# Performance work log

Hardware: AMD Instinct MI355X
Metric: run time of the kernel (lower is better)

Reference implementation:

```python
import jax, jax.numpy as jnp
import numpy as np

T, D = 8192, 256   # frames, feature dim
P, K = 64, 128     # phone vocabulary, centers per phone


def setup_inputs() -> dict:
    key = jax.random.key(0)
    k1, k2, k3 = jax.random.split(key, 3)
    h = jax.random.normal(k1, (T, D), dtype=jnp.float32)
    centers = jax.random.normal(k2, (P, K, D), dtype=jnp.float32)
    phones = jax.random.randint(k3, (T,), 0, P, dtype=jnp.int64)
    return {"h": h, "centers": centers, "phones": phones}


def reference(h, centers, phones):
    """Per-phone 1-NN retrieval: for each frame t, find nearest center in the
    pool for phones[t] and return that center (anonymized feature).
    centers: [P, K, D] padded table replacing the (pattern, phone, gender) dict.
    """
    c = centers[phones]                                # [T, K, D] irregular gather
    # squared euclidean distance; ||h_t||^2 is constant per row -> omit for argmin
    d2 = jnp.sum(c * c, axis=-1) - 2.0 * jnp.einsum("td,tkd->tk", h, c)  # [T, K]
    idx = jnp.argmin(d2, axis=-1)                      # [T]
    h_anon = jnp.take_along_axis(c, idx[:, None, None], axis=1)[:, 0, :]  # [T, D]
    return h_anon
```

## Files before the change

kernel.cpp:

```cpp
#include <hip/hip_runtime.h>

#define T_FRAMES 8192
#define D_DIM    256
#define P_PHONES 64
#define K_CENT   128
#define TILE_F   32
#define MAX_SLOTS 1024

#define WS_NORMS  0
#define WS_FIDX   32768
#define WS_DESC   65536

__global__ __launch_bounds__(1024) void qr_prep_kernel(const float* __restrict__ centers,
                                                       const int* __restrict__ phones,
                                                       float* __restrict__ norms,
                                                       int* __restrict__ fidx,
                                                       int4* __restrict__ desc) {
    const int b   = blockIdx.x;
    const int tid = threadIdx.x;

    if (b > 0) {
        const int gwave = (b - 1) * 16 + (tid >> 6);
        const int lane  = tid & 63;
        const float4 cv = ((const float4*)(centers + (size_t)gwave * D_DIM))[lane];
        float s = cv.x * cv.x + cv.y * cv.y + cv.z * cv.z + cv.w * cv.w;
#pragma unroll
        for (int off = 32; off; off >>= 1) s += __shfl_xor(s, off, 64);
        if (lane == 0) norms[gwave] = s;
        return;
    }

    __shared__ int hist[P_PHONES];
    __shared__ int offp[P_PHONES];
    if (tid < P_PHONES) hist[tid] = 0;
    for (int i = tid; i < MAX_SLOTS; i += 1024) desc[i] = make_int4(0, 0, 0, 0);
    __syncthreads();
    for (int i = tid; i < T_FRAMES; i += 1024) atomicAdd(&hist[phones[i]], 1);
    __syncthreads();

    if (tid < 64) {
        const int c = hist[tid];
        int x = c;
#pragma unroll
        for (int off = 1; off < 64; off <<= 1) {
            int y = __shfl_up(x, off, 64);
            if (tid >= off) x += y;
        }
        const int fbase = x - c;
        offp[tid] = fbase;
        const int nt = (c + TILE_F - 1) / TILE_F;

        const int srcp = ((tid & 7) << 3) | (tid >> 3);
        const int ntq  = __shfl(nt, srcp, 64);
        int y2 = ntq;
#pragma unroll
        for (int off = 1; off < 64; off <<= 1) {
            int z = __shfl_up(y2, off, 64);
            if (tid >= off) y2 += z;
        }
        const int excl   = y2 - ntq;
        const int clbase = __shfl(excl, tid & 56, 64);
        const int within = excl - clbase;
        const int fb_q   = __shfl(fbase, srcp, 64);
        const int c_q    = __shfl(c, srcp, 64);
        const int r      = tid >> 3;
        for (int j = 0; j < ntq; ++j) {
            const int slot = r + 8 * (within + j);
            if (slot < MAX_SLOTS)
                desc[slot] = make_int4(srcp, fb_q + j * TILE_F,
                                       min(TILE_F, c_q - j * TILE_F), 0);
        }
    }
    __syncthreads();

    for (int i = tid; i < T_FRAMES; i += 1024) {
        const int p = phones[i];
        fidx[atomicAdd(&offp[p], 1)] = i;
    }
}

#define DOT4(a, hv, cv) do { a = fmaf((hv).x, (cv).x, a); a = fmaf((hv).y, (cv).y, a); \
                             a = fmaf((hv).z, (cv).z, a); a = fmaf((hv).w, (cv).w, a); } while (0)

__global__ __launch_bounds__(256, 4) void qr_main_kernel(const float* __restrict__ h,
                                                         const float* __restrict__ centers,
                                                         const float* __restrict__ norms,
                                                         const int* __restrict__ fidx,
                                                         const int4* __restrict__ desc,
                                                         float* __restrict__ out) {
    const int4 dsc = desc[blockIdx.x];
    const int fcnt = dsc.z;
    if (fcnt == 0) return;
    const int p = dsc.x, fstart = dsc.y;

    const int tid  = threadIdx.x;
    const int wave = tid >> 6;
    const int lane = tid & 63;
    const int cg   = lane >> 3;
    const int fg   = lane & 7;

    __shared__ float4 hT[64][TILE_F];
    __shared__ unsigned long long keys[4][TILE_F];
    __shared__ int widx[TILE_F];

    {
        const int fr = tid & 31;
        const int wc = (tid >> 5) * 8;
        const int fi = fidx[fstart + min(fr, fcnt - 1)];
        const float4* hr = (const float4*)(h + (size_t)fi * D_DIM);
#pragma unroll
        for (int j = 0; j < 8; ++j) hT[wc + j][fr] = hr[wc + j];
    }
    __syncthreads();

    const float* c0 = centers + ((size_t)p * K_CENT + wave * 32 + cg) * D_DIM;

    float acc[4][4];
#pragma unroll
    for (int a = 0; a < 4; ++a)
#pragma unroll
        for (int bb = 0; bb < 4; ++bb) acc[a][bb] = 0.0f;

    for (int w = 0; w < 64; w += 2) {
        float4 cv[2][4], hv[2][4];
#pragma unroll
        for (int u = 0; u < 2; ++u)
#pragma unroll
            for (int j = 0; j < 4; ++j)
                cv[u][j] = ((const float4*)(c0 + (size_t)j * 8 * D_DIM))[w + u];
#pragma unroll
        for (int u = 0; u < 2; ++u)
#pragma unroll
            for (int i = 0; i < 4; ++i)
                hv[u][i] = hT[w + u][fg + 8 * i];
#pragma unroll
        for (int u = 0; u < 2; ++u)
#pragma unroll
            for (int i = 0; i < 4; ++i)
#pragma unroll
                for (int j = 0; j < 4; ++j)
                    DOT4(acc[i][j], hv[u][i], cv[u][j]);
    }

    const float* nrm = norms + p * K_CENT + wave * 32 + cg;
    unsigned long long kf[4];
#pragma unroll
    for (int i = 0; i < 4; ++i) {
        float best = 3.0e38f; int bj = 0;
#pragma unroll
        for (int j = 0; j < 4; ++j) {
            const float d2 = nrm[8 * j] - 2.0f * acc[i][j];
            if (d2 < best) { best = d2; bj = j; }
        }
        unsigned ub = __float_as_uint(best);
        ub = (ub & 0x80000000u) ? ~ub : (ub | 0x80000000u);
        kf[i] = ((unsigned long long)ub << 32) | (unsigned)(wave * 32 + cg + 8 * bj);
    }
#pragma unroll
    for (int i = 0; i < 4; ++i) {
        unsigned long long o;
        o = __shfl_xor(kf[i], 8, 64);  kf[i] = o < kf[i] ? o : kf[i];
        o = __shfl_xor(kf[i], 16, 64); kf[i] = o < kf[i] ? o : kf[i];
        o = __shfl_xor(kf[i], 32, 64); kf[i] = o < kf[i] ? o : kf[i];
    }
    if (cg == 0) {
#pragma unroll
        for (int i = 0; i < 4; ++i) keys[wave][fg + 8 * i] = kf[i];
    }
    __syncthreads();

    if (tid < TILE_F) {
        unsigned long long m = keys[0][tid];
#pragma unroll
        for (int wv = 1; wv < 4; ++wv) { const unsigned long long o = keys[wv][tid]; m = o < m ? o : m; }
        widx[tid] = (int)(m & 0xFFu);
    }
    __syncthreads();

    const int r2 = tid >> 3;
    const int q2 = tid & 7;
    if (r2 < fcnt) {
        const int fo = fidx[fstart + r2];
        const float4* src = (const float4*)(centers + ((size_t)p * K_CENT + widx[r2]) * D_DIM);
        float4* dst = (float4*)(out + (size_t)fo * D_DIM);
#pragma unroll
        for (int j = 0; j < 8; ++j) dst[q2 + 8 * j] = src[q2 + 8 * j];
    }
}

extern "C" void kernel_launch(void* const* d_in, const int* in_sizes, int n_in,
                              void* d_out, int out_size, void* d_ws, size_t ws_size,
                              hipStream_t stream) {
    const float* h       = (const float*)d_in[0];
    const float* centers = (const float*)d_in[1];
    const int*   phones  = (const int*)d_in[2];
    float*       out     = (float*)d_out;

    char* ws = (char*)d_ws;
    float* norms = (float*)(ws + WS_NORMS);
    int*   fidx  = (int*)(ws + WS_FIDX);
    int4*  desc  = (int4*)(ws + WS_DESC);

    qr_prep_kernel<<<513, 1024, 0, stream>>>(centers, phones, norms, fidx, desc);
    qr_main_kernel<<<MAX_SLOTS, 256, 0, stream>>>(h, centers, norms, fidx, desc, out);
}
```

Measured before the change: 109.2 us.

## Split the distance dot product across two D-halves with 512-thread blocks

Each block now runs 8 waves instead of 4. The waves are split into two groups that each handle half of the feature dimension, which halves the serial FMA loop per thread. The second half's partial dot products go into shared memory and the first half adds them before the argmin. The h-tile load and the output copy are spread over the larger block. This is meant to cut per-block latency and add parallelism, at the cost of extra shared memory (a 16KB partial buffer), another barrier, and possibly lower occupancy.

```diff
diff --git a/kernel.cpp b/kernel.cpp
--- a/kernel.cpp
+++ b/kernel.cpp
@@ -82,7 +82,7 @@
 #define DOT4(a, hv, cv) do { a = fmaf((hv).x, (cv).x, a); a = fmaf((hv).y, (cv).y, a); \
                              a = fmaf((hv).z, (cv).z, a); a = fmaf((hv).w, (cv).w, a); } while (0)
 
-__global__ __launch_bounds__(256, 4) void qr_main_kernel(const float* __restrict__ h,
+__global__ __launch_bounds__(512, 4) void qr_main_kernel(const float* __restrict__ h,
                                                          const float* __restrict__ centers,
                                                          const float* __restrict__ norms,
                                                          const int* __restrict__ fidx,
@@ -94,26 +94,30 @@
     const int p = dsc.x, fstart = dsc.y;
 
     const int tid  = threadIdx.x;
-    const int wave = tid >> 6;
+    const int wv   = tid >> 6;
+    const int dh   = wv >> 2;
+    const int cq   = wv & 3;
     const int lane = tid & 63;
     const int cg   = lane >> 3;
     const int fg   = lane & 7;
 
     __shared__ float4 hT[64][TILE_F];
+    __shared__ float  part[4][TILE_F * 32];
     __shared__ unsigned long long keys[4][TILE_F];
     __shared__ int widx[TILE_F];
 
     {
         const int fr = tid & 31;
-        const int wc = (tid >> 5) * 8;
+        const int wc = (tid >> 5) << 2;
         const int fi = fidx[fstart + min(fr, fcnt - 1)];
         const float4* hr = (const float4*)(h + (size_t)fi * D_DIM);
 #pragma unroll
-        for (int j = 0; j < 8; ++j) hT[wc + j][fr] = hr[wc + j];
-    }
-    __syncthreads();
-
-    const float* c0 = centers + ((size_t)p * K_CENT + wave * 32 + cg) * D_DIM;
+        for (int j = 0; j < 4; ++j) hT[wc + j][fr] = hr[wc + j];
+    }
+    __syncthreads();
+
+    const float* c0 = centers + ((size_t)p * K_CENT + cq * 32 + cg) * D_DIM + dh * 128;
+    const int wbase = dh * 32;
 
     float acc[4][4];
 #pragma unroll
@@ -121,7 +125,7 @@
 #pragma unroll
         for (int bb = 0; bb < 4; ++bb) acc[a][bb] = 0.0f;
 
-    for (int w = 0; w < 64; w += 2) {
+    for (int w = 0; w < 32; w += 2) {
         float4 cv[2][4], hv[2][4];
 #pragma unroll
         for (int u = 0; u < 2; ++u)
@@ -132,7 +136,7 @@
         for (int u = 0; u < 2; ++u)
 #pragma unroll
             for (int i = 0; i < 4; ++i)
-                hv[u][i] = hT[w + u][fg + 8 * i];
+                hv[u][i] = hT[wbase + w + u][fg + 8 * i];
 #pragma unroll
         for (int u = 0; u < 2; ++u)
 #pragma unroll
@@ -142,49 +146,66 @@
                     DOT4(acc[i][j], hv[u][i], cv[u][j]);
     }
 
-    const float* nrm = norms + p * K_CENT + wave * 32 + cg;
-    unsigned long long kf[4];
-#pragma unroll
-    for (int i = 0; i < 4; ++i) {
-        float best = 3.0e38f; int bj = 0;
-#pragma unroll
-        for (int j = 0; j < 4; ++j) {
-            const float d2 = nrm[8 * j] - 2.0f * acc[i][j];
-            if (d2 < best) { best = d2; bj = j; }
-        }
-        unsigned ub = __float_as_uint(best);
-        ub = (ub & 0x80000000u) ? ~ub : (ub | 0x80000000u);
-        kf[i] = ((unsigned long long)ub << 32) | (unsigned)(wave * 32 + cg + 8 * bj);
-    }
-#pragma unroll
-    for (int i = 0; i < 4; ++i) {
-        unsigned long long o;
-        o = __shfl_xor(kf[i], 8, 64);  kf[i] = o < kf[i] ? o : kf[i];
-        o = __shfl_xor(kf[i], 16, 64); kf[i] = o < kf[i] ? o : kf[i];
-        o = __shfl_xor(kf[i], 32, 64); kf[i] = o < kf[i] ? o : kf[i];
-    }
-    if (cg == 0) {
-#pragma unroll
-        for (int i = 0; i < 4; ++i) keys[wave][fg + 8 * i] = kf[i];
+    if (dh == 1) {
+#pragma unroll
+        for (int i = 0; i < 4; ++i)
+#pragma unroll
+            for (int j = 0; j < 4; ++j)
+                part[cq][(fg + 8 * i) * 32 + cg + 8 * j] = acc[i][j];
+    }
+    __syncthreads();
+
+    if (dh == 0) {
+#pragma unroll
+        for (int i = 0; i < 4; ++i)
+#pragma unroll
+            for (int j = 0; j < 4; ++j)
+                acc[i][j] += part[cq][(fg + 8 * i) * 32 + cg + 8 * j];
+
+        const float* nrm = norms + p * K_CENT + cq * 32 + cg;
+        unsigned long long kf[4];
+#pragma unroll
+        for (int i = 0; i < 4; ++i) {
+            float best = 3.0e38f; int bj = 0;
+#pragma unroll
+            for (int j = 0; j < 4; ++j) {
+                const float d2 = nrm[8 * j] - 2.0f * acc[i][j];
+                if (d2 < best) { best = d2; bj = j; }
+            }
+            unsigned ub = __float_as_uint(best);
+            ub = (ub & 0x80000000u) ? ~ub : (ub | 0x80000000u);
+            kf[i] = ((unsigned long long)ub << 32) | (unsigned)(cq * 32 + cg + 8 * bj);
+        }
+#pragma unroll
+        for (int i = 0; i < 4; ++i) {
+            unsigned long long o;
+            o = __shfl_xor(kf[i], 8, 64);  kf[i] = o < kf[i] ? o : kf[i];
+            o = __shfl_xor(kf[i], 16, 64); kf[i] = o < kf[i] ? o : kf[i];
+            o = __shfl_xor(kf[i], 32, 64); kf[i] = o < kf[i] ? o : kf[i];
+        }
+        if (cg == 0) {
+#pragma unroll
+            for (int i = 0; i < 4; ++i) keys[cq][fg + 8 * i] = kf[i];
+        }
     }
     __syncthreads();
 
     if (tid < TILE_F) {
         unsigned long long m = keys[0][tid];
 #pragma unroll
-        for (int wv = 1; wv < 4; ++wv) { const unsigned long long o = keys[wv][tid]; m = o < m ? o : m; }
+        for (int q = 1; q < 4; ++q) { const unsigned long long o = keys[q][tid]; m = o < m ? o : m; }
         widx[tid] = (int)(m & 0xFFu);
     }
     __syncthreads();
 
-    const int r2 = tid >> 3;
-    const int q2 = tid & 7;
+    const int r2 = tid >> 4;
+    const int q2 = tid & 15;
     if (r2 < fcnt) {
         const int fo = fidx[fstart + r2];
         const float4* src = (const float4*)(centers + ((size_t)p * K_CENT + widx[r2]) * D_DIM);
         float4* dst = (float4*)(out + (size_t)fo * D_DIM);
 #pragma unroll
-        for (int j = 0; j < 8; ++j) dst[q2 + 8 * j] = src[q2 + 8 * j];
+        for (int j = 0; j < 4; ++j) dst[q2 + 16 * j] = src[q2 + 16 * j];
     }
 }
 
@@ -202,5 +223,5 @@
     int4*  desc  = (int4*)(ws + WS_DESC);
 
     qr_prep_kernel<<<513, 1024, 0, stream>>>(centers, phones, norms, fidx, desc);
-    qr_main_kernel<<<MAX_SLOTS, 256, 0, stream>>>(h, centers, norms, fidx, desc, out);
+    qr_main_kernel<<<MAX_SLOTS, 512, 0, stream>>>(h, centers, norms, fidx, desc, out);
 }
```

After: 102.6 us. 6.0% less time.
